# Kernel optimization log

Measured on AMD Instinct MI355X. Metric: run time of the kernel, lower is better.

Reference implementation:

```python
import jax, jax.numpy as jnp
import numpy as np

EMBED = 768
HEADS = 12
HEAD_DIM = EMBED // HEADS
HIDDEN = 4 * EMBED
EPS = 1e-5


def _layernorm(x, g, b):
    mu = jnp.mean(x, axis=-1, keepdims=True)
    var = jnp.var(x, axis=-1, keepdims=True)
    return (x - mu) * jax.lax.rsqrt(var + EPS) * g + b


def setup_inputs() -> dict:
    key = jax.random.key(0)
    ks = jax.random.split(key, 12)
    s_e = 1.0 / np.sqrt(EMBED)
    s_h = 1.0 / np.sqrt(HIDDEN)
    return {
        "x": jax.random.normal(ks[0], (2, 2048, EMBED), dtype=jnp.float32),
        "ln1_g": jnp.ones((EMBED,), jnp.float32),
        "ln1_b": jnp.zeros((EMBED,), jnp.float32),
        "qkv_w": jax.random.uniform(ks[1], (EMBED, 3 * EMBED), jnp.float32, -s_e, s_e),
        "qkv_b": jax.random.uniform(ks[2], (3 * EMBED,), jnp.float32, -s_e, s_e),
        "proj_w": jax.random.uniform(ks[3], (EMBED, EMBED), jnp.float32, -s_e, s_e),
        "proj_b": jax.random.uniform(ks[4], (EMBED,), jnp.float32, -s_e, s_e),
        "ln2_g": jnp.ones((EMBED,), jnp.float32),
        "ln2_b": jnp.zeros((EMBED,), jnp.float32),
        "fc1_w": jax.random.uniform(ks[5], (EMBED, HIDDEN), jnp.float32, -s_e, s_e),
        "fc1_b": jax.random.uniform(ks[6], (HIDDEN,), jnp.float32, -s_e, s_e),
        "fc2_w": jax.random.uniform(ks[7], (HIDDEN, EMBED), jnp.float32, -s_h, s_h),
        "fc2_b": jax.random.uniform(ks[8], (EMBED,), jnp.float32, -s_h, s_h),
    }


def reference(x, ln1_g, ln1_b, qkv_w, qkv_b, proj_w, proj_b,
              ln2_g, ln2_b, fc1_w, fc1_b, fc2_w, fc2_b):
    B, L, C = x.shape
    scale = HEAD_DIM ** -0.5

    # --- attention sublayer (pre-LN) ---
    h = _layernorm(x, ln1_g, ln1_b)
    qkv = h @ qkv_w + qkv_b                       # [B, L, 3C]
    qkv = qkv.reshape(B, L, 3, HEADS, HEAD_DIM)
    q = jnp.transpose(qkv[:, :, 0], (0, 2, 1, 3))  # [B, H, L, D]
    k = jnp.transpose(qkv[:, :, 1], (0, 2, 1, 3))
    v = jnp.transpose(qkv[:, :, 2], (0, 2, 1, 3))
    attn = jnp.einsum('bhqd,bhkd->bhqk', q, k) * scale  # [B, H, L, L]
    attn = jax.nn.softmax(attn, axis=-1)
    out = jnp.einsum('bhqk,bhkd->bhqd', attn, v)  # [B, H, L, D]
    out = jnp.transpose(out, (0, 2, 1, 3)).reshape(B, L, C)
    x = x + (out @ proj_w + proj_b)

    # --- FFN sublayer (pre-LN) ---
    h = _layernorm(x, ln2_g, ln2_b)
    h = jax.nn.gelu(h @ fc1_w + fc1_b, approximate=False)
    x = x + (h @ fc2_w + fc2_b)
    return x
```

## Files before the change

kernel.cpp:

```cpp
#include <hip/hip_runtime.h>
#include <hip/hip_bf16.h>
#include <math.h>

#define EMBED   768
#define NHEADS  12
#define HD      64
#define HIDDEN  3072
#define SEQ     2048
#define BATCH   2
#define ROWS    (BATCH*SEQ)

#define QSCALE  0.1803368801111204f

typedef __bf16 bf16_t;
typedef __attribute__((ext_vector_type(8))) __bf16 bf16x8;
typedef __attribute__((ext_vector_type(4))) float f32x4;

static __device__ __forceinline__ f32x4 mfma16(bf16x8 a, bf16x8 b, f32x4 c) {
  return __builtin_amdgcn_mfma_f32_16x16x32_bf16(a, b, c, 0, 0, 0);
}

typedef __attribute__((address_space(1))) const void gas_void;
typedef __attribute__((address_space(3))) void las_void;
static __device__ __forceinline__ void gll16(const void* g, void* l) {
  __builtin_amdgcn_global_load_lds((gas_void*)g, (las_void*)l, 16, 0, 0);
}

__global__ __launch_bounds__(256) void ln_kernel(
    const float* __restrict__ x, const float* __restrict__ g,
    const float* __restrict__ bt, bf16_t* __restrict__ out)
{
  int row = blockIdx.x;
  int tid = threadIdx.x;
  const float* xr = x + (size_t)row * EMBED;
  float v0 = xr[tid], v1 = xr[tid + 256], v2 = xr[tid + 512];
  float s  = v0 + v1 + v2;
  float s2 = v0*v0 + v1*v1 + v2*v2;
  #pragma unroll
  for (int o = 32; o >= 1; o >>= 1) {
    s  += __shfl_xor(s,  o, 64);
    s2 += __shfl_xor(s2, o, 64);
  }
  __shared__ float red[8];
  int wave = tid >> 6, lane = tid & 63;
  if (lane == 0) { red[wave] = s; red[wave + 4] = s2; }
  __syncthreads();
  s  = red[0] + red[1] + red[2] + red[3];
  s2 = red[4] + red[5] + red[6] + red[7];
  float mu  = s * (1.0f / EMBED);
  float var = s2 * (1.0f / EMBED) - mu * mu;
  float rs  = rsqrtf(var + 1e-5f);
  bf16_t* orow = out + (size_t)row * EMBED;
  orow[tid]       = (bf16_t)((v0 - mu) * rs * g[tid]       + bt[tid]);
  orow[tid + 256] = (bf16_t)((v1 - mu) * rs * g[tid + 256] + bt[tid + 256]);
  orow[tid + 512] = (bf16_t)((v2 - mu) * rs * g[tid + 512] + bt[tid + 512]);
}

__global__ __launch_bounds__(256) void transpose_cast(
    const float* __restrict__ in, bf16_t* __restrict__ out, int R, int C)
{
  __shared__ float tile[32][33];
  int c0 = blockIdx.x * 32, r0 = blockIdx.y * 32;
  int tx = threadIdx.x & 31, ty = threadIdx.x >> 5;
  #pragma unroll
  for (int p = 0; p < 4; ++p) {
    int r = ty + p * 8;
    tile[r][tx] = in[(size_t)(r0 + r) * C + c0 + tx];
  }
  __syncthreads();
  #pragma unroll
  for (int p = 0; p < 4; ++p) {
    int cc = ty + p * 8;
    out[(size_t)(c0 + cc) * R + r0 + tx] = (bf16_t)tile[tx][cc];
  }
}

__global__ __launch_bounds__(256) void v_transpose(
    const bf16_t* __restrict__ qkv, bf16_t* __restrict__ vt)
{
  __shared__ bf16_t tile[64][68];
  int bh = blockIdx.y;
  int b = bh / NHEADS, h = bh % NHEADS;
  int l0 = blockIdx.x * 64;
  int t = threadIdx.x;
  int dx = (t & 15) * 4;
  int ly = t >> 4;
  #pragma unroll
  for (int p = 0; p < 4; ++p) {
    int l = ly + p * 16;
    const bf16_t* src = qkv + (size_t)(b * SEQ + l0 + l) * 2304 + 1536 + h * HD + dx;
    *(uint2*)&tile[l][dx] = *(const uint2*)src;
  }
  __syncthreads();
  int lx = (t & 15) * 4;
  int dy = t >> 4;
  #pragma unroll
  for (int p = 0; p < 4; ++p) {
    int d = dy + p * 16;
    union { bf16_t h4[4]; uint2 u; } tmp;
    #pragma unroll
    for (int i = 0; i < 4; ++i) tmp.h4[i] = tile[lx + i][d];
    *(uint2*)&vt[((size_t)bh * HD + d) * SEQ + l0 + lx] = tmp.u;
  }
}

template<int MODE, int BN>
__global__ __launch_bounds__(256) void gemm_kernel(
    const bf16_t* __restrict__ A, const bf16_t* __restrict__ WT,
    const float* __restrict__ bias, const float* __restrict__ res,
    void* __restrict__ outp, int N, int K)
{
  constexpr int JT = BN / 32;
  __shared__ bf16_t As[128 * 64];
  __shared__ bf16_t Bs[BN * 64];
  int tid = threadIdx.x;
  int lane = tid & 63, wave = tid >> 6;
  int l15 = lane & 15, quad = lane >> 4;
  int wm = wave >> 1, wn = wave & 1;
  int m0 = blockIdx.y * 128, n0 = blockIdx.x * BN;

  f32x4 acc[4][JT];
  #pragma unroll
  for (int i = 0; i < 4; ++i)
    #pragma unroll
    for (int j = 0; j < JT; ++j)
      acc[i][j] = (f32x4){0.f, 0.f, 0.f, 0.f};

  int grow = lane >> 3;
  int gcol = ((lane & 7) ^ grow) * 8;
  const bf16_t* abase = A  + (size_t)(m0 + wave * 32 + grow) * K + gcol;
  const bf16_t* bbase = WT + (size_t)(n0 + wave * (BN / 4) + grow) * K + gcol;
  int swk = l15 & 7;

  for (int k0 = 0; k0 < K; k0 += 64) {
    #pragma unroll
    for (int a = 0; a < 4; ++a)
      gll16(abase + (size_t)a * 8 * K + k0, &As[(wave * 32 + a * 8) * 64]);
    #pragma unroll
    for (int a = 0; a < BN / 32; ++a)
      gll16(bbase + (size_t)a * 8 * K + k0, &Bs[(wave * (BN / 4) + a * 8) * 64]);
    __syncthreads();

    #pragma unroll
    for (int g = 0; g < 2; ++g) {
      bf16x8 af[4], bfr[JT];
      #pragma unroll
      for (int i = 0; i < 4; ++i)
        af[i] = *(const bf16x8*)
            &As[(wm * 64 + i * 16 + l15) * 64 + (((g * 4 + quad) ^ swk) * 8)];
      #pragma unroll
      for (int j = 0; j < JT; ++j)
        bfr[j] = *(const bf16x8*)
            &Bs[(wn * (BN / 2) + j * 16 + l15) * 64 + (((g * 4 + quad) ^ swk) * 8)];
      #pragma unroll
      for (int i = 0; i < 4; ++i)
        #pragma unroll
        for (int j = 0; j < JT; ++j)
          acc[i][j] = mfma16(af[i], bfr[j], acc[i][j]);
    }
    __syncthreads();
  }

  #pragma unroll
  for (int i = 0; i < 4; ++i) {
    int mbase = m0 + wm * 64 + i * 16 + quad * 4;
    #pragma unroll
    for (int j = 0; j < JT; ++j) {
      int n = n0 + wn * (BN / 2) + j * 16 + l15;
      float bn = bias[n];
      #pragma unroll
      for (int r = 0; r < 4; ++r) {
        size_t idx = (size_t)(mbase + r) * N + n;
        float v = acc[i][j][r] + bn;
        if (MODE == 1) v = 0.5f * v * (1.0f + erff(v * 0.70710678118654752f));
        if (MODE == 3 && n < 768) v *= QSCALE;
        if (MODE == 2) {
          v += res[idx];
          ((float*)outp)[idx] = v;
        } else {
          ((bf16_t*)outp)[idx] = (bf16_t)v;
        }
      }
    }
  }
}

__global__ __launch_bounds__(256, 3) void attn_kernel(
    const bf16_t* __restrict__ qkv, const bf16_t* __restrict__ vt,
    bf16_t* __restrict__ attnout)
{
  __attribute__((aligned(16))) __shared__ bf16_t smem[8192 + 8192 + 10240];
  __shared__ float dsumf[4][64];

  int qt = blockIdx.x, h = blockIdx.y, b = blockIdx.z;
  int tid = threadIdx.x;
  int wave = tid >> 6, lane = tid & 63;
  int l15 = lane & 15, quad = lane >> 4;
  int q0 = qt * 64;
  int bh = b * NHEADS + h;

  bf16_t* kt  = smem + wave * 2048;
  bf16_t* vtl = smem + 8192 + wave * 2048;
  bf16_t* pt  = smem + 16384 + wave * 2560;

  bf16x8 aq[4][2];
  #pragma unroll
  for (int qi = 0; qi < 4; ++qi) {
    const bf16_t* qrow = qkv + (size_t)(b * SEQ + q0 + qi * 16 + l15) * 2304
                             + h * HD + quad * 8;
    aq[qi][0] = *(const bf16x8*)qrow;
    aq[qi][1] = *(const bf16x8*)(qrow + 32);
  }

  f32x4 accO[4][4];
  #pragma unroll
  for (int qi = 0; qi < 4; ++qi)
    #pragma unroll
    for (int t2 = 0; t2 < 4; ++t2)
      accO[qi][t2] = (f32x4){0.f, 0.f, 0.f, 0.f};
  float lpart[4][4] = {};

  int krow_l = lane >> 3;
  int kchunk = ((lane & 7) ^ krow_l) * 8;
  const bf16_t* ksrc0 = qkv + (size_t)(b * SEQ + wave * 32 + krow_l) * 2304
                            + 768 + h * HD + kchunk;
  int vrow_l = lane >> 2;
  int vchunk = ((lane & 3) ^ (vrow_l & 3)) * 8;
  const bf16_t* vsrc0 = vt + ((size_t)bh * HD + vrow_l) * SEQ + wave * 32 + vchunk;
  int swk = l15 & 7, swv = l15 & 3;

  for (int kv0 = 0; kv0 < SEQ; kv0 += 128) {
    const bf16_t* ks = ksrc0 + (size_t)kv0 * 2304;
    gll16(ks,                       kt);
    gll16(ks + (size_t) 8 * 2304,   kt + 512);
    gll16(ks + (size_t)16 * 2304,   kt + 1024);
    gll16(ks + (size_t)24 * 2304,   kt + 1536);
    const bf16_t* vs = vsrc0 + kv0;
    gll16(vs,                       vtl);
    gll16(vs + (size_t)16 * SEQ,    vtl + 512);
    gll16(vs + (size_t)32 * SEQ,    vtl + 1024);
    gll16(vs + (size_t)48 * SEQ,    vtl + 1536);
    __asm__ volatile("s_waitcnt vmcnt(0)" ::: "memory");

    bf16x8 bk[2][2];
    #pragma unroll
    for (int t = 0; t < 2; ++t)
      #pragma unroll
      for (int f = 0; f < 2; ++f)
        bk[t][f] = *(const bf16x8*)
            &kt[(t * 16 + l15) * 64 + (((f * 4 + quad) ^ swk) * 8)];

    #pragma unroll
    for (int qi = 0; qi < 4; ++qi) {
      #pragma unroll
      for (int t = 0; t < 2; ++t) {
        f32x4 s = (f32x4){0.f, 0.f, 0.f, 0.f};
        s = mfma16(aq[qi][0], bk[t][0], s);
        s = mfma16(aq[qi][1], bk[t][1], s);
        #pragma unroll
        for (int r = 0; r < 4; ++r) {
          float pv = exp2f(s[r]);
          lpart[qi][r] += pv;
          pt[(qi * 16 + quad * 4 + r) * 40 + t * 16 + l15] = (bf16_t)pv;
        }
      }
    }

    #pragma unroll
    for (int qi = 0; qi < 4; ++qi) {
      bf16x8 ap = *(const bf16x8*)&pt[(qi * 16 + l15) * 40 + quad * 8];
      #pragma unroll
      for (int t2 = 0; t2 < 4; ++t2) {
        bf16x8 bv = *(const bf16x8*)
            &vtl[(t2 * 16 + l15) * 32 + ((quad ^ swv) * 8)];
        accO[qi][t2] = mfma16(ap, bv, accO[qi][t2]);
      }
    }
  }

  #pragma unroll
  for (int qi = 0; qi < 4; ++qi)
    #pragma unroll
    for (int r = 0; r < 4; ++r) {
      float l = lpart[qi][r];
      l += __shfl_xor(l, 1, 64);
      l += __shfl_xor(l, 2, 64);
      l += __shfl_xor(l, 4, 64);
      l += __shfl_xor(l, 8, 64);
      lpart[qi][r] = l;
    }
  if (l15 == 0) {
    #pragma unroll
    for (int qi = 0; qi < 4; ++qi)
      #pragma unroll
      for (int r = 0; r < 4; ++r)
        dsumf[wave][qi * 16 + quad * 4 + r] = lpart[qi][r];
  }
  __syncthreads();

  float* slabf = (float*)smem;
  int rq = lane >> 3;
  int d0 = (lane & 7) * 8;

  #pragma unroll
  for (int pass = 0; pass < 2; ++pass) {
    if (pass) __syncthreads();
    #pragma unroll
    for (int qi2 = 0; qi2 < 2; ++qi2) {
      int qi = pass * 2 + qi2;
      #pragma unroll
      for (int t2 = 0; t2 < 4; ++t2)
        #pragma unroll
        for (int r = 0; r < 4; ++r)
          slabf[wave * 2048 + (qi2 * 16 + quad * 4 + r) * 64 + t2 * 16 + l15]
              = accO[qi][t2][r];
    }
    __syncthreads();
    int q_loc = wave * 8 + rq;
    f32x4 o0 = (f32x4){0.f,0.f,0.f,0.f}, o1 = (f32x4){0.f,0.f,0.f,0.f};
    #pragma unroll
    for (int sw = 0; sw < 4; ++sw) {
      o0 += *(const f32x4*)&slabf[sw * 2048 + q_loc * 64 + d0];
      o1 += *(const f32x4*)&slabf[sw * 2048 + q_loc * 64 + d0 + 4];
    }
    int q_abs = pass * 32 + q_loc;
    float den = dsumf[0][q_abs] + dsumf[1][q_abs] + dsumf[2][q_abs] + dsumf[3][q_abs];
    float inv = 1.0f / den;
    bf16_t ob[8];
    #pragma unroll
    for (int j = 0; j < 4; ++j) {
      ob[j]     = (bf16_t)(o0[j] * inv);
      ob[j + 4] = (bf16_t)(o1[j] * inv);
    }
    *(uint4*)&attnout[(size_t)(b * SEQ + q0 + q_abs) * EMBED + h * HD + d0]
        = *(const uint4*)ob;
  }
}

extern "C" void kernel_launch(void* const* d_in, const int* in_sizes, int n_in,
                              void* d_out, int out_size, void* d_ws, size_t ws_size,
                              hipStream_t stream) {
  (void)in_sizes; (void)n_in; (void)out_size; (void)ws_size;
  const float* x      = (const float*)d_in[0];
  const float* ln1_g  = (const float*)d_in[1];
  const float* ln1_b  = (const float*)d_in[2];
  const float* qkv_w  = (const float*)d_in[3];
  const float* qkv_b  = (const float*)d_in[4];
  const float* proj_w = (const float*)d_in[5];
  const float* proj_b = (const float*)d_in[6];
  const float* ln2_g  = (const float*)d_in[7];
  const float* ln2_b  = (const float*)d_in[8];
  const float* fc1_w  = (const float*)d_in[9];
  const float* fc1_b  = (const float*)d_in[10];
  const float* fc2_w  = (const float*)d_in[11];
  const float* fc2_b  = (const float*)d_in[12];
  float* out = (float*)d_out;

  char* p = (char*)d_ws;
  bf16_t* wqkvT  = (bf16_t*)p; p += (size_t)2304 * 768 * 2;
  bf16_t* wprojT = (bf16_t*)p; p += (size_t)768 * 768 * 2;
  bf16_t* wfc1T  = (bf16_t*)p; p += (size_t)3072 * 768 * 2;
  bf16_t* wfc2T  = (bf16_t*)p; p += (size_t)768 * 3072 * 2;
  bf16_t* hbuf   = (bf16_t*)p; p += (size_t)ROWS * 768 * 2;
  bf16_t* qkv    = (bf16_t*)p;
  bf16_t* hid    = (bf16_t*)p; p += (size_t)ROWS * 3072 * 2;
  bf16_t* vt     = (bf16_t*)p; p += (size_t)BATCH * NHEADS * HD * SEQ * 2;
  bf16_t* attno  = (bf16_t*)p; p += (size_t)ROWS * 768 * 2;

  transpose_cast<<<dim3(2304/32, 768/32),  256, 0, stream>>>(qkv_w,  wqkvT,  768,  2304);
  transpose_cast<<<dim3(768/32,  768/32),  256, 0, stream>>>(proj_w, wprojT, 768,  768);
  transpose_cast<<<dim3(3072/32, 768/32),  256, 0, stream>>>(fc1_w,  wfc1T,  768,  3072);
  transpose_cast<<<dim3(768/32,  3072/32), 256, 0, stream>>>(fc2_w,  wfc2T,  3072, 768);

  ln_kernel<<<ROWS, 256, 0, stream>>>(x, ln1_g, ln1_b, hbuf);
  gemm_kernel<3,128><<<dim3(2304/128, ROWS/128), 256, 0, stream>>>(
      hbuf, wqkvT, qkv_b, nullptr, qkv, 2304, 768);
  v_transpose<<<dim3(SEQ/64, BATCH*NHEADS), 256, 0, stream>>>(qkv, vt);
  attn_kernel<<<dim3(SEQ/64, NHEADS, BATCH), 256, 0, stream>>>(qkv, vt, attno);
  gemm_kernel<2,64><<<dim3(768/64, ROWS/128), 256, 0, stream>>>(
      attno, wprojT, proj_b, x, out, 768, 768);

  ln_kernel<<<ROWS, 256, 0, stream>>>(out, ln2_g, ln2_b, hbuf);
  gemm_kernel<1,128><<<dim3(3072/128, ROWS/128), 256, 0, stream>>>(
      hbuf, wfc1T, fc1_b, nullptr, hid, 3072, 768);
  gemm_kernel<2,64><<<dim3(768/64, ROWS/128), 256, 0, stream>>>(
      hid, wfc2T, fc2_b, out, out, 768, 3072);
}
```

Before: 311.0 us.

## Double-buffer attention K/V loads, transpose score MFMA, and swizzle GEMM block order

```diff
diff --git a/kernel.cpp b/kernel.cpp
--- a/kernel.cpp
+++ b/kernel.cpp
@@ -117,7 +117,12 @@
   int lane = tid & 63, wave = tid >> 6;
   int l15 = lane & 15, quad = lane >> 4;
   int wm = wave >> 1, wn = wave & 1;
-  int m0 = blockIdx.y * 128, n0 = blockIdx.x * BN;
+
+  int Nn = N / BN;
+  int lin = blockIdx.x;
+  int bm = (lin & 7) + 8 * ((lin >> 3) / Nn);
+  int bn = (lin >> 3) % Nn;
+  int m0 = bm * 128, n0 = bn * BN;
 
   f32x4 acc[4][JT];
   #pragma unroll
@@ -167,11 +172,11 @@
     #pragma unroll
     for (int j = 0; j < JT; ++j) {
       int n = n0 + wn * (BN / 2) + j * 16 + l15;
-      float bn = bias[n];
+      float bn_ = bias[n];
       #pragma unroll
       for (int r = 0; r < 4; ++r) {
         size_t idx = (size_t)(mbase + r) * N + n;
-        float v = acc[i][j][r] + bn;
+        float v = acc[i][j][r] + bn_;
         if (MODE == 1) v = 0.5f * v * (1.0f + erff(v * 0.70710678118654752f));
         if (MODE == 3 && n < 768) v *= QSCALE;
         if (MODE == 2) {
@@ -185,11 +190,11 @@
   }
 }
 
-__global__ __launch_bounds__(256, 3) void attn_kernel(
+__global__ __launch_bounds__(256, 2) void attn_kernel(
     const bf16_t* __restrict__ qkv, const bf16_t* __restrict__ vt,
     bf16_t* __restrict__ attnout)
 {
-  __attribute__((aligned(16))) __shared__ bf16_t smem[8192 + 8192 + 10240];
+  __attribute__((aligned(16))) __shared__ bf16_t smem[4 * 8192 + 4 * 640];
   __shared__ float dsumf[4][64];
 
   int qt = blockIdx.x, h = blockIdx.y, b = blockIdx.z;
@@ -199,17 +204,16 @@
   int q0 = qt * 64;
   int bh = b * NHEADS + h;
 
-  bf16_t* kt  = smem + wave * 2048;
-  bf16_t* vtl = smem + 8192 + wave * 2048;
-  bf16_t* pt  = smem + 16384 + wave * 2560;
-
-  bf16x8 aq[4][2];
+  bf16_t* wbase = smem + wave * 8192;
+  bf16_t* pt    = smem + 32768 + wave * 640;
+
+  bf16x8 bq[4][2];
   #pragma unroll
   for (int qi = 0; qi < 4; ++qi) {
     const bf16_t* qrow = qkv + (size_t)(b * SEQ + q0 + qi * 16 + l15) * 2304
                              + h * HD + quad * 8;
-    aq[qi][0] = *(const bf16x8*)qrow;
-    aq[qi][1] = *(const bf16x8*)(qrow + 32);
+    bq[qi][0] = *(const bf16x8*)qrow;
+    bq[qi][1] = *(const bf16x8*)(qrow + 32);
   }
 
   f32x4 accO[4][4];
@@ -218,7 +222,7 @@
     #pragma unroll
     for (int t2 = 0; t2 < 4; ++t2)
       accO[qi][t2] = (f32x4){0.f, 0.f, 0.f, 0.f};
-  float lpart[4][4] = {};
+  float lpart[4] = {0.f, 0.f, 0.f, 0.f};
 
   int krow_l = lane >> 3;
   int kchunk = ((lane & 7) ^ krow_l) * 8;
@@ -227,74 +231,86 @@
   int vrow_l = lane >> 2;
   int vchunk = ((lane & 3) ^ (vrow_l & 3)) * 8;
   const bf16_t* vsrc0 = vt + ((size_t)bh * HD + vrow_l) * SEQ + wave * 32 + vchunk;
-  int swk = l15 & 7, swv = l15 & 3;
-
-  for (int kv0 = 0; kv0 < SEQ; kv0 += 128) {
-    const bf16_t* ks = ksrc0 + (size_t)kv0 * 2304;
-    gll16(ks,                       kt);
-    gll16(ks + (size_t) 8 * 2304,   kt + 512);
-    gll16(ks + (size_t)16 * 2304,   kt + 1024);
-    gll16(ks + (size_t)24 * 2304,   kt + 1536);
-    const bf16_t* vs = vsrc0 + kv0;
-    gll16(vs,                       vtl);
-    gll16(vs + (size_t)16 * SEQ,    vtl + 512);
-    gll16(vs + (size_t)32 * SEQ,    vtl + 1024);
-    gll16(vs + (size_t)48 * SEQ,    vtl + 1536);
-    __asm__ volatile("s_waitcnt vmcnt(0)" ::: "memory");
-
-    bf16x8 bk[2][2];
+
+  constexpr int NIT = SEQ / 128;
+
+  {
+    const bf16_t* ks = ksrc0;
+    const bf16_t* vs = vsrc0;
+    bf16_t* kb = wbase;
+    bf16_t* vb = wbase + 2048;
+    #pragma unroll
+    for (int p = 0; p < 4; ++p) {
+      gll16(ks + (size_t)(p * 8) * 2304, kb + p * 512);
+      gll16(vs + (size_t)(p * 16) * SEQ, vb + p * 512);
+    }
+  }
+
+  int cb = 0;
+  for (int it = 0; it < NIT; ++it) {
+    {
+      int kvn = ((it + 1) & (NIT - 1)) * 128;
+      const bf16_t* ks = ksrc0 + (size_t)kvn * 2304;
+      const bf16_t* vs = vsrc0 + kvn;
+      bf16_t* kb = wbase + (cb ^ 1) * 4096;
+      bf16_t* vb = kb + 2048;
+      #pragma unroll
+      for (int p = 0; p < 4; ++p) {
+        gll16(ks + (size_t)(p * 8) * 2304, kb + p * 512);
+        gll16(vs + (size_t)(p * 16) * SEQ, vb + p * 512);
+      }
+    }
+    __asm__ volatile("s_waitcnt vmcnt(8)" ::: "memory");
+
+    const bf16_t* kb = wbase + cb * 4096;
+    const bf16_t* vb = kb + 2048;
+
+    bf16x8 ak[2][2];
     #pragma unroll
     for (int t = 0; t < 2; ++t)
       #pragma unroll
       for (int f = 0; f < 2; ++f)
-        bk[t][f] = *(const bf16x8*)
-            &kt[(t * 16 + l15) * 64 + (((f * 4 + quad) ^ swk) * 8)];
+        ak[t][f] = *(const bf16x8*)
+            &kb[(t * 16 + l15) * 64 + (((f * 4 + quad) ^ (l15 & 7)) * 8)];
+
+    bf16x8 bv[4];
+    #pragma unroll
+    for (int t2 = 0; t2 < 4; ++t2)
+      bv[t2] = *(const bf16x8*)
+          &vb[(t2 * 16 + l15) * 32 + ((quad ^ (l15 & 3)) * 8)];
 
     #pragma unroll
     for (int qi = 0; qi < 4; ++qi) {
       #pragma unroll
       for (int t = 0; t < 2; ++t) {
         f32x4 s = (f32x4){0.f, 0.f, 0.f, 0.f};
-        s = mfma16(aq[qi][0], bk[t][0], s);
-        s = mfma16(aq[qi][1], bk[t][1], s);
+        s = mfma16(ak[t][0], bq[qi][0], s);
+        s = mfma16(ak[t][1], bq[qi][1], s);
+        union { bf16_t b4[4]; uint2 u; } pk;
+        float ls = 0.f;
         #pragma unroll
         for (int r = 0; r < 4; ++r) {
           float pv = exp2f(s[r]);
-          lpart[qi][r] += pv;
-          pt[(qi * 16 + quad * 4 + r) * 40 + t * 16 + l15] = (bf16_t)pv;
+          ls += pv;
+          pk.b4[r] = (bf16_t)pv;
         }
+        lpart[qi] += ls;
+        *(uint2*)&pt[l15 * 40 + t * 16 + quad * 4] = pk.u;
       }
-    }
-
-    #pragma unroll
-    for (int qi = 0; qi < 4; ++qi) {
-      bf16x8 ap = *(const bf16x8*)&pt[(qi * 16 + l15) * 40 + quad * 8];
-      #pragma unroll
-      for (int t2 = 0; t2 < 4; ++t2) {
-        bf16x8 bv = *(const bf16x8*)
-            &vtl[(t2 * 16 + l15) * 32 + ((quad ^ swv) * 8)];
-        accO[qi][t2] = mfma16(ap, bv, accO[qi][t2]);
-      }
-    }
-  }
-
-  #pragma unroll
-  for (int qi = 0; qi < 4; ++qi)
-    #pragma unroll
-    for (int r = 0; r < 4; ++r) {
-      float l = lpart[qi][r];
-      l += __shfl_xor(l, 1, 64);
-      l += __shfl_xor(l, 2, 64);
-      l += __shfl_xor(l, 4, 64);
-      l += __shfl_xor(l, 8, 64);
-      lpart[qi][r] = l;
-    }
-  if (l15 == 0) {
-    #pragma unroll
-    for (int qi = 0; qi < 4; ++qi)
-      #pragma unroll
-      for (int r = 0; r < 4; ++r)
-        dsumf[wave][qi * 16 + quad * 4 + r] = lpart[qi][r];
+      bf16x8 ap = *(const bf16x8*)&pt[l15 * 40 + quad * 8];
+      #pragma unroll
+      for (int t2 = 0; t2 < 4; ++t2)
+        accO[qi][t2] = mfma16(ap, bv[t2], accO[qi][t2]);
+    }
+    cb ^= 1;
+  }
+
+  #pragma unroll
+  for (int qi = 0; qi < 4; ++qi) {
+    float l = lpart[qi];
+    l += __shfl_xor(l, 16, 64);
+    l += __shfl_xor(l, 32, 64);
+    if (quad == 0) dsumf[wave][qi * 16 + l15] = l;
   }
   __syncthreads();
 
@@ -373,16 +389,16 @@
   transpose_cast<<<dim3(768/32,  3072/32), 256, 0, stream>>>(fc2_w,  wfc2T,  3072, 768);
 
   ln_kernel<<<ROWS, 256, 0, stream>>>(x, ln1_g, ln1_b, hbuf);
-  gemm_kernel<3,128><<<dim3(2304/128, ROWS/128), 256, 0, stream>>>(
+  gemm_kernel<3,128><<<32 * (2304/128), 256, 0, stream>>>(
       hbuf, wqkvT, qkv_b, nullptr, qkv, 2304, 768);
   v_transpose<<<dim3(SEQ/64, BATCH*NHEADS), 256, 0, stream>>>(qkv, vt);
   attn_kernel<<<dim3(SEQ/64, NHEADS, BATCH), 256, 0, stream>>>(qkv, vt, attno);
-  gemm_kernel<2,64><<<dim3(768/64, ROWS/128), 256, 0, stream>>>(
+  gemm_kernel<2,64><<<32 * (768/64), 256, 0, stream>>>(
       attno, wprojT, proj_b, x, out, 768, 768);
 
   ln_kernel<<<ROWS, 256, 0, stream>>>(out, ln2_g, ln2_b, hbuf);
-  gemm_kernel<1,128><<<dim3(3072/128, ROWS/128), 256, 0, stream>>>(
+  gemm_kernel<1,128><<<32 * (3072/128), 256, 0, stream>>>(
       hbuf, wfc1T, fc1_b, nullptr, hid, 3072, 768);
-  gemm_kernel<2,64><<<dim3(768/64, ROWS/128), 256, 0, stream>>>(
+  gemm_kernel<2,64><<<32 * (768/64), 256, 0, stream>>>(
       hid, wfc2T, fc2_b, out, out, 768, 3072);
 }
```

Result: faster. 303.4 us (-2.4%).
